# Performance work log

Measured on AMD Instinct MI355X. Metric: run time of the kernel, lower is better.

The kernel has to match this reference:

```python
import jax, jax.numpy as jnp
import numpy as np

N = 50000
NEG_SLOPE = 0.01  # F.leaky_relu default


def gcn_conv(x, edge_index, edge_weight, W, b):
    """PyG GCNConv: h = x @ W; symmetric-normalized aggregation with self-loops; + bias."""
    n = x.shape[0]
    h = x @ W                                # [N, out]
    src, dst = edge_index[0], edge_index[1]
    # degree includes self-loop weight 1.0 per node
    deg = jax.ops.segment_sum(edge_weight, dst, num_segments=n) + 1.0
    dinv = jax.lax.rsqrt(deg)                # deg >= 1, no zero guard needed
    norm = dinv[src] * edge_weight * dinv[dst]
    agg = jax.ops.segment_sum(norm[:, None] * h[src], dst, num_segments=n)
    agg = agg + (dinv * dinv)[:, None] * h   # self-loop contribution: deg^-1 * h_i
    return agg + b


def setup_inputs() -> dict:
    key = jax.random.key(0)
    ks = jax.random.split(key, 24)
    in_size, hid, out = 256, 64, 32
    E = 800000
    d = {}
    for i, nm in enumerate(["x1", "x2", "x3"]):
        d[nm] = jax.random.normal(ks[i], (N, in_size), dtype=jnp.float32)
    for i, nm in enumerate(["edge_index1", "edge_index2", "edge_index3"]):
        d[nm] = jax.random.randint(ks[3 + i], (2, E), 0, N, dtype=jnp.int32)
    for i, nm in enumerate(["edge_weight1", "edge_weight2", "edge_weight3"]):
        d[nm] = jax.random.uniform(ks[6 + i], (E,), dtype=jnp.float32)
    s_in = 1.0 / np.sqrt(in_size)
    s_h = 1.0 / np.sqrt(hid)
    for i, nm in enumerate(["W1", "W2", "W3"]):
        d[nm] = jax.random.uniform(ks[9 + i], (in_size, hid), minval=-s_in, maxval=s_in, dtype=jnp.float32)
    for i, nm in enumerate(["b1", "b2", "b3"]):
        d[nm] = jax.random.uniform(ks[12 + i], (hid,), minval=-s_in, maxval=s_in, dtype=jnp.float32)
    d["fc_w"] = jax.random.uniform(ks[15], (hid, 1), minval=-s_h, maxval=s_h, dtype=jnp.float32)
    d["fc_b"] = jax.random.uniform(ks[16], (1,), minval=-s_h, maxval=s_h, dtype=jnp.float32)
    for i, nm in enumerate(["W11", "W22", "W33"]):
        d[nm] = jax.random.uniform(ks[17 + i], (hid, out), minval=-s_h, maxval=s_h, dtype=jnp.float32)
    for i, nm in enumerate(["b11", "b22", "b33"]):
        d[nm] = jax.random.uniform(ks[20 + i], (out,), minval=-s_h, maxval=s_h, dtype=jnp.float32)
    return d


def reference(x1, x2, x3, edge_index1, edge_index2, edge_index3,
              edge_weight1, edge_weight2, edge_weight3,
              W1, W2, W3, b1, b2, b3, fc_w, fc_b,
              W11, W22, W33, b11, b22, b33):
    # branch embeddings (dropout is identity in eval mode)
    e1 = jax.nn.relu(gcn_conv(x1, edge_index1, edge_weight1, W1, b1))
    e2 = jax.nn.relu(gcn_conv(x2, edge_index2, edge_weight2, W2, b2))
    e3 = jax.nn.relu(gcn_conv(x3, edge_index3, edge_weight3, W3, b3))
    # attention coefficients
    c1 = jnp.exp(jax.nn.leaky_relu(e1 @ fc_w + fc_b, NEG_SLOPE))  # [N,1]
    c2 = jnp.exp(jax.nn.leaky_relu(e2 @ fc_w + fc_b, NEG_SLOPE))
    c3 = jnp.exp(jax.nn.leaky_relu(e3 @ fc_w + fc_b, NEG_SLOPE))
    cd = c1 + c2 + c3
    coef1, coef2, coef3 = c1 / cd, c2 / cd, c3 / cd
    combined = e1 * coef1 + e2 * coef2 + e3 * coef3
    out1 = gcn_conv(combined, edge_index1, edge_weight1, W11, b11)
    out2 = gcn_conv(combined, edge_index2, edge_weight2, W22, b22)
    out3 = gcn_conv(combined, edge_index3, edge_weight3, W33, b33)
    return (out1 + out2 + out3, coef1, coef2, coef3)
```

## Files before the change

### kernel.cpp

```cpp
#include <hip/hip_runtime.h>
#include <hip/hip_fp16.h>
#include <math.h>

#define NN    50000
#define INF_  256
#define HID   64
#define OUTF  32
#define EE    800000
#define TOTN  (3 * NN)
#define NBKT  196
#define NBIN  (3 * NBKT)
#define CBLK  391
#define NCNT  (3 * CBLK)
#define GB    1563
#define NGEMM (3 * GB)
#define MAXB  5120
#define NBLK  12500

typedef unsigned long long u64;
typedef unsigned int       u32;
typedef unsigned short     u16;
typedef _Float16           f16;
typedef f16   f16x8 __attribute__((ext_vector_type(8)));
typedef f16   f16x4 __attribute__((ext_vector_type(4)));
typedef float f32x4 __attribute__((ext_vector_type(4)));

__global__ __launch_bounds__(256) void k_prep(
        const float* __restrict__ W1, const float* __restrict__ W2, const float* __restrict__ W3,
        f16* __restrict__ Wt2, u32* __restrict__ bin_cursor) {
    int blk = blockIdx.x, t = threadIdx.x;
    if (blk == 3) {
        for (int i = t; i < NBIN; i += 256) bin_cursor[i] = 0;
        return;
    }
    const float* W = (blk == 0) ? W1 : (blk == 1) ? W2 : W3;
    f16* wt = Wt2 + blk * 16384;
    for (int idx = t; idx < 16384; idx += 256) {
        int e    = idx & 7;
        int lane = (idx >> 3) & 63;
        int kt   = (idx >> 9) & 7;
        int c    = idx >> 12;
        int col  = c * 16 + (lane & 15);
        int k    = kt * 32 + ((lane >> 4) << 3) + e;
        wt[idx] = (f16)W[k * HID + col];
    }
}

__global__ __launch_bounds__(256) void k_scatgemm(
        const int* __restrict__ ei1, const int* __restrict__ ei2, const int* __restrict__ ei3,
        const float* __restrict__ ew1, const float* __restrict__ ew2, const float* __restrict__ ew3,
        u32* __restrict__ bin_cursor, u64* __restrict__ bucketed,
        const float* __restrict__ x1, const float* __restrict__ x2, const float* __restrict__ x3,
        const f16* __restrict__ Wt2, __half* __restrict__ h) {
    __shared__ __align__(16) char smem[20480];
    int bid = blockIdx.x;
    int q = bid / 5, r = bid - q * 5;
    int t = threadIdx.x;

    if (r == 4) {
        u64* ent  = (u64*)smem;
        u32* acnt = (u32*)(smem + 16384);
        u32* ascn = acnt + 256;
        u32* acur = ascn + 256;
        u32* adel = acur + 256;
        int cb  = q;
        int br  = cb / CBLK;
        int blk = cb - br * CBLK;
        const int*   ei = (br == 0) ? ei1 : (br == 1) ? ei2 : ei3;
        const float* ew = (br == 0) ? ew1 : (br == 1) ? ew2 : ew3;
        acnt[t] = 0; acur[t] = 0;
        __syncthreads();
        int e0 = blk * 2048;
        int tot = EE - e0; if (tot > 2048) tot = 2048; if (tot < 0) tot = 0;
        u32 dstv[8];
#pragma unroll
        for (int k = 0; k < 8; ++k) {
            int e = e0 + k * 256 + t;
            if (e < EE) {
                dstv[k] = (u32)ei[EE + e];
                atomicAdd(&acnt[dstv[k] >> 8], 1u);
            }
        }
        __syncthreads();
        ascn[t] = acnt[t];
        __syncthreads();
        for (int d = 1; d < 256; d <<= 1) {
            u32 v = (t >= d) ? ascn[t - d] : 0;
            __syncthreads();
            ascn[t] += v;
            __syncthreads();
        }
        if (t < NBKT) {
            u32 cnt = acnt[t];
            u32 base = cnt ? atomicAdd(&bin_cursor[br * NBKT + t], cnt) : 0;
            adel[t] = (u32)(br * NBKT + t) * MAXB + base - (ascn[t] - acnt[t]);
        }
        __syncthreads();
#pragma unroll
        for (int k = 0; k < 8; ++k) {
            int e = e0 + k * 256 + t;
            if (e < EE) {
                u32 dst = dstv[k];
                u32 src = (u32)ei[e];
                u32 bkt = dst >> 8;
                u16 w16 = __half_as_ushort(__float2half(ew[e]));
                u32 rnk = atomicAdd(&acur[bkt], 1u);
                u32 ls  = ascn[bkt] - acnt[bkt] + rnk;
                ent[ls] = ((u64)bkt << 48) | ((u64)w16 << 32)
                        | ((u64)src << 8) | (u64)(dst & 0xffu);
            }
        }
        __syncthreads();
        for (int i = t; i < tot; i += 256) {
            u64 ev = ent[i];
            u32 bkt = (u32)(ev >> 48) & 0xffu;
            bucketed[adel[bkt] + i] = ev;
        }
        return;
    }

    int gid = q * 4 + r;
    if (gid >= NGEMM) return;
    f16 (*xl)[264] = reinterpret_cast<f16(*)[264]>(smem);
    int b = gid / GB;
    int row_base = (gid - b * GB) * 32;
    const float4* x4 = reinterpret_cast<const float4*>((b == 0) ? x1 : (b == 1) ? x2 : x3);
    const f16* wt2 = Wt2 + b * 16384;
    __half* hb = h + (size_t)b * NN * HID;

    float4 v[8];
#pragma unroll
    for (int j = 0; j < 8; ++j) {
        int flat = j * 256 + t;
        int gr = row_base + (flat >> 6);
        v[j] = (gr < NN) ? x4[(size_t)row_base * 64 + flat]
                         : make_float4(0.f, 0.f, 0.f, 0.f);
    }
#pragma unroll
    for (int j = 0; j < 8; ++j) {
        int flat = j * 256 + t;
        int rr = flat >> 6, c4 = flat & 63;
        f16x4 p = {(f16)v[j].x, (f16)v[j].y, (f16)v[j].z, (f16)v[j].w};
        *(f16x4*)&xl[rr][c4 * 4] = p;
    }
    __syncthreads();

    int w      = t >> 6;
    int lane   = t & 63;
    int lrow   = lane & 15;
    int lk     = (lane >> 4) * 8;
    int rloc   = (w & 1) * 16;
    int ctile0 = (w >> 1) * 2;
    int arow   = rloc + lrow;

    f32x4 acc[2] = {{0,0,0,0},{0,0,0,0}};
#pragma unroll
    for (int kt = 0; kt < 8; ++kt) {
        f16x8 af = *(const f16x8*)&xl[arow][kt * 32 + lk];
#pragma unroll
        for (int ci = 0; ci < 2; ++ci) {
            int c = ctile0 + ci;
            f16x8 bf = *(const f16x8*)&wt2[((c * 8 + kt) * 64 + lane) * 8];
            acc[ci] = __builtin_amdgcn_mfma_f32_16x16x32_f16(af, bf, acc[ci], 0, 0, 0);
        }
    }
    int orow0 = row_base + rloc + ((lane >> 4) << 2);
#pragma unroll
    for (int ci = 0; ci < 2; ++ci) {
#pragma unroll
        for (int i = 0; i < 4; ++i) {
            int row = orow0 + i;
            if (row < NN)
                hb[(size_t)row * HID + (ctile0 + ci) * 16 + lrow] = __float2half(acc[ci][i]);
        }
    }
}

__global__ __launch_bounds__(256) void k_bucket(
        const u64* __restrict__ bucketed, const u32* __restrict__ bin_cursor,
        u32* __restrict__ nodeinfo, float* __restrict__ dinv,
        u32* __restrict__ csr, __half* __restrict__ h) {
    __shared__ u32   scnt[256];
    __shared__ float swsum[256];
    __shared__ u32   scur[256];
    __shared__ u32   sscan[256];
    __shared__ float sdiv[256];
    __shared__ u32   lcsr[MAXB];
    int bin = blockIdx.x;
    int br  = bin / NBKT;
    int bkt = bin - br * NBKT;
    int t = threadIdx.x;
    u32 base = (u32)bin * MAXB;
    u32 ecnt = bin_cursor[bin];
    scnt[t] = 0; swsum[t] = 0.f; scur[t] = 0;
    __syncthreads();
    for (u32 i = t; i < ecnt; i += 256) {
        u64 e = bucketed[base + i];
        u32 dl = (u32)e & 0xffu;
        atomicAdd(&scnt[dl], 1u);
        atomicAdd(&swsum[dl], __half2float(__ushort_as_half((u16)((e >> 32) & 0xffffu))));
    }
    __syncthreads();
    sscan[t] = scnt[t];
    __syncthreads();
    for (int d = 1; d < 256; d <<= 1) {
        u32 v = (t >= d) ? sscan[t - d] : 0;
        __syncthreads();
        sscan[t] += v;
        __syncthreads();
    }
    u32 lstart = sscan[t] - scnt[t];
    float d = rsqrtf(1.0f + swsum[t]);
    sdiv[t] = d;
    int n = bkt * 256 + t;
    if (n < NN) {
        int gi = br * NN + n;
        nodeinfo[gi] = ((base + lstart) << 10) | scnt[t];
        dinv[gi]     = d;
    }
    __syncthreads();
    for (u32 i = t; i < ecnt; i += 256) {
        u64 e = bucketed[base + i];
        u32 dl  = (u32)e & 0xffu;
        u32 src = (u32)(e >> 8) & 0xffffu;
        u32 w16 = (u32)(e >> 32) & 0xffffu;
        u32 rnk = atomicAdd(&scur[dl], 1u);
        u32 ls  = sscan[dl] - scnt[dl];
        lcsr[ls + rnk] = (w16 << 16) | src;
    }
    __syncthreads();
    for (u32 i = t; i < ecnt; i += 256) csr[base + i] = lcsr[i];

    int nrows = NN - bkt * 256; if (nrows > 256) nrows = 256;
    u32* hrow = (u32*)(h + ((size_t)br * NN + (size_t)bkt * 256) * HID);
    for (int i = t; i < nrows * 32; i += 256) {
        float dd = sdiv[i >> 5];
        __half2 hv = *(__half2*)&hrow[i];
        float2 v = __half22float2(hv);
        __half2 rr = __float22half2_rn(make_float2(v.x * dd, v.y * dd));
        hrow[i] = *(u32*)&rr;
    }
}

__global__ __launch_bounds__(256) void k_agg1(
        const u32* __restrict__ csr, const u32* __restrict__ nodeinfo,
        const float* __restrict__ dinv,
        const float* __restrict__ b1, const float* __restrict__ b2, const float* __restrict__ b3,
        const __half* __restrict__ h, __half* __restrict__ e) {
    int bid = blockIdx.x;
    int br  = bid / NBLK;
    int nb  = bid - br * NBLK;
    int t   = threadIdx.x;
    int f2  = t & 31;
    int eo  = (t >> 5) & 1;
    int sub = __builtin_amdgcn_readfirstlane(t >> 6);
    int n   = nb * 4 + sub;

    const float* bi = (br == 0) ? b1 : (br == 1) ? b2 : b3;
    const __half2* hb2 = (const __half2*)(h + (size_t)br * NN * HID);
    int i   = br * NN + n;
    u32 inf = nodeinfo[i];
    int cc  = (int)(inf & 1023u);
    int st  = (int)(inf >> 10);
    float d = dinv[i];
    float2 hs = __half22float2(hb2[(size_t)n * 32 + f2]);

    float ax = 0.f, ay = 0.f;
    int cm1 = cc - 1;
    for (int j = 0; j < cc; j += 16) {
        u32 ee[8]; __half2 vv[8];
#pragma unroll
        for (int u = 0; u < 8; ++u) {
            int jj = j + 2 * u + eo;
            ee[u] = csr[st + (jj < cm1 ? jj : cm1)];
            if (jj >= cc) ee[u] &= 0xffffu;
        }
#pragma unroll
        for (int u = 0; u < 8; ++u)
            vv[u] = hb2[(size_t)(ee[u] & 0xffff) * 32 + f2];
#pragma unroll
        for (int u = 0; u < 8; ++u) {
            float w = __half2float(__ushort_as_half((u16)(ee[u] >> 16)));
            float2 v = __half22float2(vv[u]);
            ax = fmaf(w, v.x, ax);
            ay = fmaf(w, v.y, ay);
        }
    }
    ax += __shfl_xor(ax, 32);
    ay += __shfl_xor(ay, 32);
    float2 bv = ((const float2*)bi)[f2];
    float ex = fmaxf(bv.x + d * (hs.x + ax), 0.f);
    float ey = fmaxf(bv.y + d * (hs.y + ay), 0.f);
    if (eo == 0)
        ((__half2*)e)[((size_t)br * NN + n) * 32 + f2] = __float22half2_rn(make_float2(ex, ey));
}

__global__ __launch_bounds__(256) void k_attn(
        const __half* __restrict__ e,
        const float* __restrict__ fc_w, const float* __restrict__ fc_b,
        __half* __restrict__ comb, float* __restrict__ coef_out) {
    int t    = threadIdx.x;
    int lane = t & 63;
    int sub  = __builtin_amdgcn_readfirstlane(t >> 6);
    int half = lane >> 5;
    int f2   = lane & 31;
    int n    = blockIdx.x * 8 + sub * 2 + half;
    float2 wv = ((const float2*)fc_w)[f2];
    float fb = fc_b[0];
    const __half2* e2 = (const __half2*)e;

    float2 ev[3]; float c[3];
#pragma unroll
    for (int b = 0; b < 3; ++b) {
        ev[b] = __half22float2(e2[((size_t)b * NN + n) * 32 + f2]);
        float dd = ev[b].x * wv.x + ev[b].y * wv.y;
#pragma unroll
        for (int off = 16; off > 0; off >>= 1) dd += __shfl_xor(dd, off);
        float z = dd + fb;
        z = (z > 0.f) ? z : 0.01f * z;
        c[b] = expf(z);
    }
    float cd = c[0] + c[1] + c[2];
    float coef0 = c[0] / cd, coef1 = c[1] / cd, coef2 = c[2] / cd;
    float cx = ev[0].x * coef0 + ev[1].x * coef1 + ev[2].x * coef2;
    float cy = ev[0].y * coef0 + ev[1].y * coef1 + ev[2].y * coef2;
    ((__half2*)comb)[(size_t)n * 32 + f2] = __float22half2_rn(make_float2(cx, cy));
    if (f2 == 0) {
        coef_out[n]          = coef0;
        coef_out[NN + n]     = coef1;
        coef_out[2 * NN + n] = coef2;
    }
}

__global__ __launch_bounds__(256) void k_gemm2(
        const __half* __restrict__ comb,
        const float* __restrict__ W11, const float* __restrict__ W22, const float* __restrict__ W33,
        const float* __restrict__ dinv, __half* __restrict__ h2) {
    __shared__ float Wls[3][HID][OUTF];
    __shared__ __half cl[8][HID];
    int t = threadIdx.x;
    {
        const float4* w40 = reinterpret_cast<const float4*>(W11);
        const float4* w41 = reinterpret_cast<const float4*>(W22);
        const float4* w42 = reinterpret_cast<const float4*>(W33);
        float4* d0 = reinterpret_cast<float4*>(&Wls[0][0][0]);
        float4* d1 = reinterpret_cast<float4*>(&Wls[1][0][0]);
        float4* d2 = reinterpret_cast<float4*>(&Wls[2][0][0]);
#pragma unroll
        for (int j = 0; j < 2; ++j) {
            d0[t + j * 256] = w40[t + j * 256];
            d1[t + j * 256] = w41[t + j * 256];
            d2[t + j * 256] = w42[t + j * 256];
        }
    }
    int row0 = blockIdx.x * 8;
    ((u32*)cl)[t] = ((const u32*)(comb + (size_t)row0 * HID))[t];
    __syncthreads();

    int col = t & 31;
    int rr  = t >> 5;
    int row = row0 + rr;
    float a0 = 0.f, a1 = 0.f, a2 = 0.f;
    for (int k = 0; k < HID; ++k) {
        float cv = __half2float(cl[rr][k]);
        a0 = fmaf(cv, Wls[0][k][col], a0);
        a1 = fmaf(cv, Wls[1][k][col], a1);
        a2 = fmaf(cv, Wls[2][k][col], a2);
    }
    float d0 = dinv[row], d1 = dinv[NN + row], d2 = dinv[2 * NN + row];
    h2[(size_t)0 * NN * OUTF + (size_t)row * OUTF + col] = __float2half(a0 * d0);
    h2[(size_t)1 * NN * OUTF + (size_t)row * OUTF + col] = __float2half(a1 * d1);
    h2[(size_t)2 * NN * OUTF + (size_t)row * OUTF + col] = __float2half(a2 * d2);
}

__global__ __launch_bounds__(256) void k_agg2p(
        const u32* __restrict__ csr, const u32* __restrict__ nodeinfo,
        const float* __restrict__ dinv,
        const __half* __restrict__ h2, float* __restrict__ outp) {
    int bid = blockIdx.x;
    int br  = bid / NBLK;
    int nb  = bid - br * NBLK;
    int t   = threadIdx.x;
    int f2  = t & 15;
    int eo  = (t >> 4) & 3;
    int sub = __builtin_amdgcn_readfirstlane(t >> 6);
    int n   = nb * 4 + sub;

    int i   = br * NN + n;
    u32 inf = nodeinfo[i];
    int cc  = (int)(inf & 1023u);
    int st  = (int)(inf >> 10);
    const __half2* h2b = (const __half2*)(h2 + (size_t)br * NN * OUTF);
    float ax = 0.f, ay = 0.f;
    int cm1 = cc - 1;
    for (int j = 0; j < cc; j += 16) {
        u32 ee[4]; __half2 vv[4];
#pragma unroll
        for (int u = 0; u < 4; ++u) {
            int jj = j + 4 * u + eo;
            ee[u] = csr[st + (jj < cm1 ? jj : cm1)];
            if (jj >= cc) ee[u] &= 0xffffu;
        }
#pragma unroll
        for (int u = 0; u < 4; ++u)
            vv[u] = h2b[(size_t)(ee[u] & 0xffff) * 16 + f2];
#pragma unroll
        for (int u = 0; u < 4; ++u) {
            float w = __half2float(__ushort_as_half((u16)(ee[u] >> 16)));
            float2 v = __half22float2(vv[u]);
            ax = fmaf(w, v.x, ax);
            ay = fmaf(w, v.y, ay);
        }
    }
    ax += __shfl_xor(ax, 16); ay += __shfl_xor(ay, 16);
    ax += __shfl_xor(ax, 32); ay += __shfl_xor(ay, 32);
    float d = dinv[i];
    float2 hs = __half22float2(h2b[(size_t)n * 16 + f2]);
    if (eo == 0)
        ((float2*)outp)[((size_t)br * NN + n) * 16 + f2] =
            make_float2(d * (ax + hs.x), d * (ay + hs.y));
}

__global__ __launch_bounds__(256) void k_sum(
        const float* __restrict__ outp,
        const float* __restrict__ b11, const float* __restrict__ b22, const float* __restrict__ b33,
        float* __restrict__ out) {
    int i = blockIdx.x * 256 + threadIdx.x;
    int f2 = i & 15;
    const float2* p = (const float2*)outp;
    float2 v0 = p[i];
    float2 v1 = p[(size_t)NN * 16 + i];
    float2 v2 = p[(size_t)2 * NN * 16 + i];
    float2 bA = ((const float2*)b11)[f2];
    float2 bB = ((const float2*)b22)[f2];
    float2 bC = ((const float2*)b33)[f2];
    ((float2*)out)[i] = make_float2(v0.x + v1.x + v2.x + bA.x + bB.x + bC.x,
                                    v0.y + v1.y + v2.y + bA.y + bB.y + bC.y);
}

extern "C" void kernel_launch(void* const* d_in, const int* in_sizes, int n_in,
                              void* d_out, int out_size, void* d_ws, size_t ws_size,
                              hipStream_t stream) {
    const float* x1  = (const float*)d_in[0];
    const float* x2  = (const float*)d_in[1];
    const float* x3  = (const float*)d_in[2];
    const int*   ei1 = (const int*)d_in[3];
    const int*   ei2 = (const int*)d_in[4];
    const int*   ei3 = (const int*)d_in[5];
    const float* ew1 = (const float*)d_in[6];
    const float* ew2 = (const float*)d_in[7];
    const float* ew3 = (const float*)d_in[8];
    const float* W1  = (const float*)d_in[9];
    const float* W2  = (const float*)d_in[10];
    const float* W3  = (const float*)d_in[11];
    const float* b1  = (const float*)d_in[12];
    const float* b2  = (const float*)d_in[13];
    const float* b3  = (const float*)d_in[14];
    const float* fcw = (const float*)d_in[15];
    const float* fcb = (const float*)d_in[16];
    const float* W11 = (const float*)d_in[17];
    const float* W22 = (const float*)d_in[18];
    const float* W33 = (const float*)d_in[19];
    const float* b11 = (const float*)d_in[20];
    const float* b22 = (const float*)d_in[21];
    const float* b33 = (const float*)d_in[22];

    float* out = (float*)d_out;
    float* coef_out = out + (size_t)NN * OUTF;

    u64*   bucketed  = (u64*)d_ws;
    float* outp      = (float*)d_ws;
    u32*   csr       = (u32*)(bucketed + (size_t)NBIN * MAXB);
    u32*   bin_cursor= csr + (size_t)NBIN * MAXB;
    float* dinv      = (float*)(bin_cursor + NBIN + 4);
    u32*   nodeinfo  = (u32*)(dinv + TOTN);
    f16*   Wt2       = (f16*)(nodeinfo + TOTN);
    __half* h        = (__half*)(Wt2 + 3 * 16384);
    __half* comb     = h + (size_t)TOTN * HID;
    __half* h2       = comb + (size_t)NN * HID;
    __half* e        = h2 + (size_t)TOTN * OUTF;

    k_prep<<<dim3(4), 256, 0, stream>>>(W1, W2, W3, Wt2, bin_cursor);
    k_scatgemm<<<dim3(NCNT * 5), 256, 0, stream>>>(ei1, ei2, ei3, ew1, ew2, ew3,
                                                   bin_cursor, bucketed,
                                                   x1, x2, x3, Wt2, h);
    k_bucket<<<dim3(NBIN), 256, 0, stream>>>(bucketed, bin_cursor,
                                             nodeinfo, dinv, csr, h);

    k_agg1<<<dim3(3 * NBLK), 256, 0, stream>>>(csr, nodeinfo, dinv, b1, b2, b3, h, e);
    k_attn<<<dim3(NN / 8), 256, 0, stream>>>(e, fcw, fcb, comb, coef_out);
    k_gemm2<<<dim3(NN / 8), 256, 0, stream>>>(comb, W11, W22, W33, dinv, h2);
    k_agg2p<<<dim3(3 * NBLK), 256, 0, stream>>>(csr, nodeinfo, dinv, h2, outp);
    k_sum<<<dim3(3125), 256, 0, stream>>>(outp, b11, b22, b33, out);
}
```

Baseline: 246.9 us.

## Fuse attention into gemm2, split bucket entries, stage GEMM output stores

Merges the attention kernel and the second GEMM into one kernel, so the combined embedding stays in shared memory as fp32 instead of round-tripping through a global fp16 buffer. Replaces the 8-byte bucketed edge entries with a 4-byte word plus a 1-byte local destination, which cuts scatter and bucket traffic and lets the bucket pass copy the word straight into the CSR. Routes the first GEMM's output through shared memory so rows are written with coalesced 16-byte stores. The fused kernel does the small GEMM with a serial 64-step loop per output, and the workspace layout is reshuffled.

```diff
diff --git a/kernel.cpp b/kernel.cpp
--- a/kernel.cpp
+++ b/kernel.cpp
@@ -20,6 +20,7 @@
 typedef unsigned long long u64;
 typedef unsigned int       u32;
 typedef unsigned short     u16;
+typedef unsigned char      u8;
 typedef _Float16           f16;
 typedef f16   f16x8 __attribute__((ext_vector_type(8)));
 typedef f16   f16x4 __attribute__((ext_vector_type(4)));
@@ -49,20 +50,21 @@
 __global__ __launch_bounds__(256) void k_scatgemm(
         const int* __restrict__ ei1, const int* __restrict__ ei2, const int* __restrict__ ei3,
         const float* __restrict__ ew1, const float* __restrict__ ew2, const float* __restrict__ ew3,
-        u32* __restrict__ bin_cursor, u64* __restrict__ bucketed,
+        u32* __restrict__ bin_cursor, u32* __restrict__ bkt32, u8* __restrict__ bkt8,
         const float* __restrict__ x1, const float* __restrict__ x2, const float* __restrict__ x3,
         const f16* __restrict__ Wt2, __half* __restrict__ h) {
-    __shared__ __align__(16) char smem[20480];
+    __shared__ __align__(16) char smem[16896];
     int bid = blockIdx.x;
     int q = bid / 5, r = bid - q * 5;
     int t = threadIdx.x;
 
     if (r == 4) {
-        u64* ent  = (u64*)smem;
-        u32* acnt = (u32*)(smem + 16384);
-        u32* ascn = acnt + 256;
-        u32* acur = ascn + 256;
-        u32* adel = acur + 256;
+        u32* ent32 = (u32*)smem;
+        u16* ent16 = (u16*)(smem + 8192);
+        u32* acnt  = (u32*)(smem + 12288);
+        u32* ascn  = acnt + 256;
+        u32* acur  = ascn + 256;
+        u32* adel  = acur + 256;
         int cb  = q;
         int br  = cb / CBLK;
         int blk = cb - br * CBLK;
@@ -106,15 +108,18 @@
                 u16 w16 = __half_as_ushort(__float2half(ew[e]));
                 u32 rnk = atomicAdd(&acur[bkt], 1u);
                 u32 ls  = ascn[bkt] - acnt[bkt] + rnk;
-                ent[ls] = ((u64)bkt << 48) | ((u64)w16 << 32)
-                        | ((u64)src << 8) | (u64)(dst & 0xffu);
+                ent32[ls] = ((u32)w16 << 16) | src;
+                ent16[ls] = (u16)((bkt << 8) | (dst & 0xffu));
             }
         }
         __syncthreads();
         for (int i = t; i < tot; i += 256) {
-            u64 ev = ent[i];
-            u32 bkt = (u32)(ev >> 48) & 0xffu;
-            bucketed[adel[bkt] + i] = ev;
+            u32 v32 = ent32[i];
+            u32 v16 = ent16[i];
+            u32 bkt = v16 >> 8;
+            u32 pos = adel[bkt] + i;
+            bkt32[pos] = v32;
+            bkt8[pos]  = (u8)v16;
         }
         return;
     }
@@ -164,20 +169,24 @@
             acc[ci] = __builtin_amdgcn_mfma_f32_16x16x32_f16(af, bf, acc[ci], 0, 0, 0);
         }
     }
-    int orow0 = row_base + rloc + ((lane >> 4) << 2);
-#pragma unroll
-    for (int ci = 0; ci < 2; ++ci) {
-#pragma unroll
-        for (int i = 0; i < 4; ++i) {
-            int row = orow0 + i;
-            if (row < NN)
-                hb[(size_t)row * HID + (ctile0 + ci) * 16 + lrow] = __float2half(acc[ci][i]);
-        }
-    }
+    __syncthreads();
+    __half* hout = (__half*)smem;
+#pragma unroll
+    for (int ci = 0; ci < 2; ++ci)
+#pragma unroll
+        for (int i = 0; i < 4; ++i)
+            hout[(rloc + ((lane >> 4) << 2) + i) * 64 + (ctile0 + ci) * 16 + lrow] =
+                __float2half(acc[ci][i]);
+    __syncthreads();
+    int rowl = t >> 3;
+    int grow = row_base + rowl;
+    if (grow < NN)
+        ((float4*)(hb + (size_t)grow * HID))[t & 7] = ((const float4*)smem)[t];
 }
 
 __global__ __launch_bounds__(256) void k_bucket(
-        const u64* __restrict__ bucketed, const u32* __restrict__ bin_cursor,
+        const u32* __restrict__ bkt32, const u8* __restrict__ bkt8,
+        const u32* __restrict__ bin_cursor,
         u32* __restrict__ nodeinfo, float* __restrict__ dinv,
         u32* __restrict__ csr, __half* __restrict__ h) {
     __shared__ u32   scnt[256];
@@ -195,10 +204,10 @@
     scnt[t] = 0; swsum[t] = 0.f; scur[t] = 0;
     __syncthreads();
     for (u32 i = t; i < ecnt; i += 256) {
-        u64 e = bucketed[base + i];
-        u32 dl = (u32)e & 0xffu;
+        u32 v32 = bkt32[base + i];
+        u32 dl  = bkt8[base + i];
         atomicAdd(&scnt[dl], 1u);
-        atomicAdd(&swsum[dl], __half2float(__ushort_as_half((u16)((e >> 32) & 0xffffu))));
+        atomicAdd(&swsum[dl], __half2float(__ushort_as_half((u16)(v32 >> 16))));
     }
     __syncthreads();
     sscan[t] = scnt[t];
@@ -220,13 +229,11 @@
     }
     __syncthreads();
     for (u32 i = t; i < ecnt; i += 256) {
-        u64 e = bucketed[base + i];
-        u32 dl  = (u32)e & 0xffu;
-        u32 src = (u32)(e >> 8) & 0xffffu;
-        u32 w16 = (u32)(e >> 32) & 0xffffu;
+        u32 v32 = bkt32[base + i];
+        u32 dl  = bkt8[base + i];
         u32 rnk = atomicAdd(&scur[dl], 1u);
         u32 ls  = sscan[dl] - scnt[dl];
-        lcsr[ls + rnk] = (w16 << 16) | src;
+        lcsr[ls + rnk] = v32;
     }
     __syncthreads();
     for (u32 i = t; i < ecnt; i += 256) csr[base + i] = lcsr[i];
@@ -295,49 +302,14 @@
         ((__half2*)e)[((size_t)br * NN + n) * 32 + f2] = __float22half2_rn(make_float2(ex, ey));
 }
 
-__global__ __launch_bounds__(256) void k_attn(
+__global__ __launch_bounds__(256) void k_attn_gemm2(
         const __half* __restrict__ e,
         const float* __restrict__ fc_w, const float* __restrict__ fc_b,
-        __half* __restrict__ comb, float* __restrict__ coef_out) {
-    int t    = threadIdx.x;
-    int lane = t & 63;
-    int sub  = __builtin_amdgcn_readfirstlane(t >> 6);
-    int half = lane >> 5;
-    int f2   = lane & 31;
-    int n    = blockIdx.x * 8 + sub * 2 + half;
-    float2 wv = ((const float2*)fc_w)[f2];
-    float fb = fc_b[0];
-    const __half2* e2 = (const __half2*)e;
-
-    float2 ev[3]; float c[3];
-#pragma unroll
-    for (int b = 0; b < 3; ++b) {
-        ev[b] = __half22float2(e2[((size_t)b * NN + n) * 32 + f2]);
-        float dd = ev[b].x * wv.x + ev[b].y * wv.y;
-#pragma unroll
-        for (int off = 16; off > 0; off >>= 1) dd += __shfl_xor(dd, off);
-        float z = dd + fb;
-        z = (z > 0.f) ? z : 0.01f * z;
-        c[b] = expf(z);
-    }
-    float cd = c[0] + c[1] + c[2];
-    float coef0 = c[0] / cd, coef1 = c[1] / cd, coef2 = c[2] / cd;
-    float cx = ev[0].x * coef0 + ev[1].x * coef1 + ev[2].x * coef2;
-    float cy = ev[0].y * coef0 + ev[1].y * coef1 + ev[2].y * coef2;
-    ((__half2*)comb)[(size_t)n * 32 + f2] = __float22half2_rn(make_float2(cx, cy));
-    if (f2 == 0) {
-        coef_out[n]          = coef0;
-        coef_out[NN + n]     = coef1;
-        coef_out[2 * NN + n] = coef2;
-    }
-}
-
-__global__ __launch_bounds__(256) void k_gemm2(
-        const __half* __restrict__ comb,
         const float* __restrict__ W11, const float* __restrict__ W22, const float* __restrict__ W33,
-        const float* __restrict__ dinv, __half* __restrict__ h2) {
+        const float* __restrict__ dinv,
+        __half* __restrict__ h2, float* __restrict__ coef_out) {
     __shared__ float Wls[3][HID][OUTF];
-    __shared__ __half cl[8][HID];
+    __shared__ float cls[8][HID];
     int t = threadIdx.x;
     {
         const float4* w40 = reinterpret_cast<const float4*>(W11);
@@ -353,24 +325,51 @@
             d2[t + j * 256] = w42[t + j * 256];
         }
     }
-    int row0 = blockIdx.x * 8;
-    ((u32*)cl)[t] = ((const u32*)(comb + (size_t)row0 * HID))[t];
-    __syncthreads();
-
-    int col = t & 31;
-    int rr  = t >> 5;
-    int row = row0 + rr;
-    float a0 = 0.f, a1 = 0.f, a2 = 0.f;
-    for (int k = 0; k < HID; ++k) {
-        float cv = __half2float(cl[rr][k]);
-        a0 = fmaf(cv, Wls[0][k][col], a0);
-        a1 = fmaf(cv, Wls[1][k][col], a1);
-        a2 = fmaf(cv, Wls[2][k][col], a2);
-    }
-    float d0 = dinv[row], d1 = dinv[NN + row], d2 = dinv[2 * NN + row];
-    h2[(size_t)0 * NN * OUTF + (size_t)row * OUTF + col] = __float2half(a0 * d0);
-    h2[(size_t)1 * NN * OUTF + (size_t)row * OUTF + col] = __float2half(a1 * d1);
-    h2[(size_t)2 * NN * OUTF + (size_t)row * OUTF + col] = __float2half(a2 * d2);
+    int lane = t & 63;
+    int sub  = __builtin_amdgcn_readfirstlane(t >> 6);
+    int half = lane >> 5;
+    int f2   = lane & 31;
+    int nl   = sub * 2 + half;
+    int n    = blockIdx.x * 8 + nl;
+    float2 wv = ((const float2*)fc_w)[f2];
+    float fb = fc_b[0];
+    const __half2* e2 = (const __half2*)e;
+
+    float2 ev[3]; float c[3];
+#pragma unroll
+    for (int b = 0; b < 3; ++b) {
+        ev[b] = __half22float2(e2[((size_t)b * NN + n) * 32 + f2]);
+        float dd = ev[b].x * wv.x + ev[b].y * wv.y;
+#pragma unroll
+        for (int off = 16; off > 0; off >>= 1) dd += __shfl_xor(dd, off);
+        float z = dd + fb;
+        z = (z > 0.f) ? z : 0.01f * z;
+        c[b] = expf(z);
+    }
+    float cd = c[0] + c[1] + c[2];
+    float coef0 = c[0] / cd, coef1 = c[1] / cd, coef2 = c[2] / cd;
+    cls[nl][2 * f2]     = ev[0].x * coef0 + ev[1].x * coef1 + ev[2].x * coef2;
+    cls[nl][2 * f2 + 1] = ev[0].y * coef0 + ev[1].y * coef1 + ev[2].y * coef2;
+    if (f2 == 0) {
+        coef_out[n]          = coef0;
+        coef_out[NN + n]     = coef1;
+        coef_out[2 * NN + n] = coef2;
+    }
+    __syncthreads();
+
+    for (int idx = t; idx < 768; idx += 256) {
+        int col  = idx & 31;
+        int rem  = idx >> 5;
+        int br   = rem >> 3;
+        int rowl = rem & 7;
+        float a = 0.f;
+#pragma unroll
+        for (int k = 0; k < HID; ++k)
+            a = fmaf(cls[rowl][k], Wls[br][k][col], a);
+        int row = blockIdx.x * 8 + rowl;
+        h2[(size_t)br * NN * OUTF + (size_t)row * OUTF + col] =
+            __float2half(a * dinv[br * NN + row]);
+    }
 }
 
 __global__ __launch_bounds__(256) void k_agg2p(
@@ -468,28 +467,28 @@
     float* out = (float*)d_out;
     float* coef_out = out + (size_t)NN * OUTF;
 
-    u64*   bucketed  = (u64*)d_ws;
-    float* outp      = (float*)d_ws;
-    u32*   csr       = (u32*)(bucketed + (size_t)NBIN * MAXB);
+    u32*   bkt32     = (u32*)d_ws;
+    u8*    bkt8      = (u8*)(bkt32 + (size_t)NBIN * MAXB);
+    u32*   csr       = (u32*)(bkt8 + (size_t)NBIN * MAXB + 64);
     u32*   bin_cursor= csr + (size_t)NBIN * MAXB;
     float* dinv      = (float*)(bin_cursor + NBIN + 4);
     u32*   nodeinfo  = (u32*)(dinv + TOTN);
     f16*   Wt2       = (f16*)(nodeinfo + TOTN);
     __half* h        = (__half*)(Wt2 + 3 * 16384);
-    __half* comb     = h + (size_t)TOTN * HID;
-    __half* h2       = comb + (size_t)NN * HID;
+    __half* h2       = h + (size_t)TOTN * HID;
     __half* e        = h2 + (size_t)TOTN * OUTF;
+    float* outp      = (float*)e;
 
     k_prep<<<dim3(4), 256, 0, stream>>>(W1, W2, W3, Wt2, bin_cursor);
     k_scatgemm<<<dim3(NCNT * 5), 256, 0, stream>>>(ei1, ei2, ei3, ew1, ew2, ew3,
-                                                   bin_cursor, bucketed,
+                                                   bin_cursor, bkt32, bkt8,
                                                    x1, x2, x3, Wt2, h);
-    k_bucket<<<dim3(NBIN), 256, 0, stream>>>(bucketed, bin_cursor,
+    k_bucket<<<dim3(NBIN), 256, 0, stream>>>(bkt32, bkt8, bin_cursor,
                                              nodeinfo, dinv, csr, h);
 
     k_agg1<<<dim3(3 * NBLK), 256, 0, stream>>>(csr, nodeinfo, dinv, b1, b2, b3, h, e);
-    k_attn<<<dim3(NN / 8), 256, 0, stream>>>(e, fcw, fcb, comb, coef_out);
-    k_gemm2<<<dim3(NN / 8), 256, 0, stream>>>(comb, W11, W22, W33, dinv, h2);
+    k_attn_gemm2<<<dim3(NN / 8), 256, 0, stream>>>(e, fcw, fcb, W11, W22, W33,
+                                                   dinv, h2, coef_out);
     k_agg2p<<<dim3(3 * NBLK), 256, 0, stream>>>(csr, nodeinfo, dinv, h2, outp);
     k_sum<<<dim3(3125), 256, 0, stream>>>(outp, b11, b22, b33, out);
 }
```

New measurement: 242.6 us (median of 2 runs). About the same (-1.7%).
